# Kernel optimization log

Measured on AMD Instinct MI355X. Metric: run time of the kernel, lower is better.

## Reference

```python
import jax, jax.numpy as jnp
import numpy as np

MD = 4  # max displacement -> (2*MD+1)**2 = 81 output channels

def setup_inputs() -> dict:
    key = jax.random.key(0)
    k1, k2 = jax.random.split(key)
    B, C, H, W = 4, 128, 128, 256
    t1 = jax.random.normal(k1, (B, C, H, W), dtype=jnp.float32)
    t2 = jax.random.normal(k2, (B, C, H, W), dtype=jnp.float32)
    return {"t1": t1, "t2": t2}

def reference(t1, t2):
    # PWC-Net correlation: for each displacement (dy,dx) in [-MD,MD]^2,
    # corr[b, d, y, x] = mean_c t1[b,c,y,x] * t2[b,c,y+dy,x+dx]
    B, C, H, W = t1.shape
    t2p = jnp.pad(t2, ((0, 0), (0, 0), (MD, MD), (MD, MD)))
    outs = []
    for dy in range(2 * MD + 1):
        for dx in range(2 * MD + 1):
            shifted = t2p[:, :, dy:dy + H, dx:dx + W]  # (B,C,H,W)
            outs.append(jnp.mean(t1 * shifted, axis=1))  # (B,H,W)
    return jnp.stack(outs, axis=1)  # (B, 81, H, W)
```

## Files before the change

kernel.cpp:

```cpp
#include <hip/hip_runtime.h>

#define MD   4
#define B_   4
#define C_   128
#define H_   128
#define W_   256
#define ND   9

typedef float  float4v __attribute__((ext_vector_type(4)));
typedef float  f32x4   __attribute__((ext_vector_type(4)));
typedef short  bf16x8  __attribute__((ext_vector_type(8)));
typedef unsigned int u32;
typedef u32    u32x4   __attribute__((ext_vector_type(4)));

static __device__ __forceinline__ unsigned short f2bf(float f) {
    u32 u = __float_as_uint(f);
    u32 r = (u + 0x7fffu + ((u >> 16) & 1u)) >> 16;
    return (unsigned short)r;
}

__global__ __launch_bounds__(256, 2)
void convert_t2(const float* __restrict__ t2,
                unsigned short* __restrict__ ws) {
    const int bid = blockIdx.x;
    const int kc  = bid & 3;
    const int y   = (bid >> 2) & (H_ - 1);
    const int b   = bid >> 9;
    const int x   = threadIdx.x;
    const float* src = t2 + ((size_t)(b * C_ + kc * 32) * H_ + y) * W_ + x;
    const size_t hw = (size_t)H_ * W_;

    float f[32];
    #pragma unroll
    for (int k = 0; k < 32; ++k) f[k] = src[(size_t)k * hw];

    unsigned short* dst =
        ws + ((((size_t)(b * H_ + y)) * 4 + kc) * W_ + x) * 32;
    #pragma unroll
    for (int q = 0; q < 4; ++q) {
        u32x4 pk;
        #pragma unroll
        for (int j = 0; j < 4; ++j)
            pk[j] = (u32)f2bf(f[q * 8 + 2 * j]) |
                    ((u32)f2bf(f[q * 8 + 2 * j + 1]) << 16);
        *(u32x4*)(dst + q * 8) = pk;
    }
}

__global__ __launch_bounds__(512, 2)
void corr_mfma4(const float* __restrict__ t1,
                const unsigned short* __restrict__ ws,
                float* __restrict__ out) {
    __shared__ float scr[8][2 * 16 * 33];

    const int tid = threadIdx.x;
    const int l   = tid & 63;
    const int w   = tid >> 6;
    const int bid = blockIdx.x;
    const int xcd = bid & 7;
    const int xh  = xcd >> 2;
    const int ypq = xcd & 3;
    const int rst = bid >> 3;
    const int b   = rst >> 4;
    const int yp  = ypq * 16 + (rst & 15);
    const int y0  = yp * 2;
    const int ln  = l & 15;
    const int kg  = l >> 4;
    const int X0  = (xh * 8 + w) * 16;
    const float scale = 1.0f / (float)C_;
    const bf16x8 z8 = (bf16x8)(short)0;
    const size_t hw = (size_t)H_ * W_;

    f32x4 aA0[ND], aA1[ND], aB0[ND], aB1[ND];
    #pragma unroll
    for (int r = 0; r < ND; ++r) {
        aA0[r] = (f32x4)0.0f; aA1[r] = (f32x4)0.0f;
        aB0[r] = (f32x4)0.0f; aB1[r] = (f32x4)0.0f;
    }

    int col0 = X0 - 8 + ln;
    int col1 = X0 + 8 + ln;
    const bool ob0 = col0 < 0;
    const bool ob1 = col1 > W_ - 1;
    col0 = ob0 ? 0 : col0;
    col1 = ob1 ? W_ - 1 : col1;

    #pragma unroll
    for (int kc = 0; kc < 4; ++kc) {
        const float* aspA =
            t1 + ((size_t)(b * C_ + kc * 32 + kg * 8) * H_ + y0) * W_ + X0 + ln;
        const float* aspB = aspA + W_;
        float avA[8], avB[8];
        #pragma unroll
        for (int j = 0; j < 8; ++j) avA[j] = __builtin_nontemporal_load(aspA + (size_t)j * hw);
        #pragma unroll
        for (int j = 0; j < 8; ++j) avB[j] = __builtin_nontemporal_load(aspB + (size_t)j * hw);
        bf16x8 fA, fB;
        #pragma unroll
        for (int j = 0; j < 8; ++j) { fA[j] = (short)f2bf(avA[j]);
                                      fB[j] = (short)f2bf(avB[j]); }

        #pragma unroll
        for (int r = 0; r < ND + 1; ++r) {
            const int row = y0 + r - MD;
            if (0 <= row && row < H_) {
                const unsigned short* b_base =
                    ws + ((((size_t)(b * H_ + row)) * 4 + kc) * W_) * 32;
                bf16x8 b0 = *(const bf16x8*)(b_base + (size_t)col0 * 32 + kg * 8);
                bf16x8 b1 = *(const bf16x8*)(b_base + (size_t)col1 * 32 + kg * 8);
                b0 = ob0 ? z8 : b0;
                b1 = ob1 ? z8 : b1;
                if (r < ND) {
                    aA0[r] = __builtin_amdgcn_mfma_f32_16x16x32_bf16(fA, b0, aA0[r], 0, 0, 0);
                    aA1[r] = __builtin_amdgcn_mfma_f32_16x16x32_bf16(fA, b1, aA1[r], 0, 0, 0);
                }
                if (r >= 1) {
                    aB0[r-1] = __builtin_amdgcn_mfma_f32_16x16x32_bf16(fB, b0, aB0[r-1], 0, 0, 0);
                    aB1[r-1] = __builtin_amdgcn_mfma_f32_16x16x32_bf16(fB, b1, aB1[r-1], 0, 0, 0);
                }
            }
        }
    }

    float* sw = scr[w];

    #pragma unroll
    for (int r = 0; r < ND; ++r) {
        const int row = y0 + r - MD;
        const bool liv = (0 <= row && row < H_);
        #pragma unroll
        for (int i = 0; i < 4; ++i) {
            sw[(kg * 4 + i) * 33 + ln]       = aA0[r][i];
            sw[528 + (kg * 4 + i) * 33 + ln] = aA1[r][i];
        }
        #pragma unroll
        for (int i = 0; i < 3; ++i) {
            const int dx = i * 4 + kg;
            if (dx < ND) {
                const int m  = ln;
                const int md = m + dx;
                const int idx = (md < 12) ? (m * 33 + md + 4)
                                          : (528 + m * 33 + md - 12);
                const float v = liv ? sw[idx] * scale : 0.0f;
                __builtin_nontemporal_store(v,
                    &out[((((size_t)b * 81) + r * ND + dx) * H_ + y0) * W_ + X0 + m]);
            }
        }
    }
    #pragma unroll
    for (int r = 0; r < ND; ++r) {
        const int row = y0 + 1 + r - MD;
        const bool liv = (0 <= row && row < H_);
        #pragma unroll
        for (int i = 0; i < 4; ++i) {
            sw[(kg * 4 + i) * 33 + ln]       = aB0[r][i];
            sw[528 + (kg * 4 + i) * 33 + ln] = aB1[r][i];
        }
        #pragma unroll
        for (int i = 0; i < 3; ++i) {
            const int dx = i * 4 + kg;
            if (dx < ND) {
                const int m  = ln;
                const int md = m + dx;
                const int idx = (md < 12) ? (m * 33 + md + 4)
                                          : (528 + m * 33 + md - 12);
                const float v = liv ? sw[idx] * scale : 0.0f;
                __builtin_nontemporal_store(v,
                    &out[((((size_t)b * 81) + r * ND + dx) * H_ + (y0 + 1)) * W_ + X0 + m]);
            }
        }
    }
}

__global__ __launch_bounds__(9 * 64, 3)
void corr_fallback(const float* __restrict__ t1,
                   const float* __restrict__ t2,
                   float* __restrict__ out) {
    const int tid  = threadIdx.x;
    const int lane = tid & 63;
    const int w    = tid >> 6;
    const int bid  = blockIdx.x;
    const int swz  = (bid & 7) * 32 + (bid >> 3);
    const int yp   = swz & 63;
    const int b    = swz >> 6;
    const int y0   = yp * 2;
    const int half = lane >> 5;
    const int lx   = lane & 31;
    const int x0   = lx * 8;
    const int yrow = y0 + half;
    const int yy   = yrow + w - MD;
    const bool live = (0 <= yy) && (yy < H_);
    const int  yc  = yy < 0 ? 0 : (yy > H_ - 1 ? H_ - 1 : yy);
    const float sc = live ? (1.0f / (float)C_) : 0.0f;
    const bool lm  = (lx == 0);
    const bool rm  = (lx == 31);
    const int offL = lm ? 0 : -4;
    const int offR = rm ? 0 :  8;

    float acc[ND][8];
    #pragma unroll
    for (int dx = 0; dx < ND; ++dx)
        #pragma unroll
        for (int j = 0; j < 8; ++j) acc[dx][j] = 0.0f;

    const float* p1 = t1 + (((size_t)(b * C_)) * H_ + yrow) * W_ + x0;
    const float* p2 = t2 + (((size_t)(b * C_)) * H_ + yc  ) * W_ + x0;
    const size_t chstr = (size_t)H_ * W_;

    #pragma unroll 2
    for (int c = 0; c < C_; ++c) {
        const float* pc1 = p1 + (size_t)c * chstr;
        const float* pc2 = p2 + (size_t)c * chstr;
        const float4v a0 = *(const float4v*)(pc1);
        const float4v a1 = *(const float4v*)(pc1 + 4);
        float4v wl = *(const float4v*)(pc2 + offL);
        const float4v v0 = *(const float4v*)(pc2);
        const float4v v1 = *(const float4v*)(pc2 + 4);
        float4v wr = *(const float4v*)(pc2 + offR);
        #pragma unroll
        for (int q = 0; q < 4; ++q) {
            wl[q] = lm ? 0.0f : wl[q];
            wr[q] = rm ? 0.0f : wr[q];
        }
        float win[16];
        #pragma unroll
        for (int q = 0; q < 4; ++q) {
            win[q] = wl[q]; win[4 + q] = v0[q];
            win[8 + q] = v1[q]; win[12 + q] = wr[q];
        }
        #pragma unroll
        for (int dx = 0; dx < ND; ++dx)
            #pragma unroll
            for (int j = 0; j < 8; ++j) {
                const float aj = (j < 4) ? a0[j] : a1[j - 4];
                acc[dx][j] = fmaf(aj, win[dx + j], acc[dx][j]);
            }
    }

    #pragma unroll
    for (int dx = 0; dx < ND; ++dx) {
        float4v o0, o1;
        #pragma unroll
        for (int j = 0; j < 4; ++j) {
            o0[j] = acc[dx][j] * sc;
            o1[j] = acc[dx][4 + j] * sc;
        }
        const size_t oidx =
            (((size_t)(b * ND * ND) + w * ND + dx) * H_ + yrow) * W_ + x0;
        *(float4v*)&out[oidx]     = o0;
        *(float4v*)&out[oidx + 4] = o1;
    }
}

extern "C" void kernel_launch(void* const* d_in, const int* in_sizes, int n_in,
                              void* d_out, int out_size, void* d_ws, size_t ws_size,
                              hipStream_t stream) {
    const float* t1 = (const float*)d_in[0];
    const float* t2 = (const float*)d_in[1];
    float* out      = (float*)d_out;
    const size_t need = (size_t)B_ * H_ * 4 * W_ * 32 * sizeof(unsigned short);
    if (ws_size >= need) {
        unsigned short* ws = (unsigned short*)d_ws;
        convert_t2<<<dim3(B_ * H_ * 4), 256, 0, stream>>>(t2, ws);
        corr_mfma4<<<dim3(B_ * H_), 512, 0, stream>>>(t1, ws, out);
    } else {
        corr_fallback<<<dim3(B_ * H_ / 2), 9 * 64, 0, stream>>>(t1, t2, out);
    }
}
```

Measured before the change: 74.90 us.

## Pre-convert t1 to channel-packed bf16 alongside t2 and use regular stores

The conversion kernel now packs both t1 and t2 into channel-interleaved bf16 workspace buffers. The correlation kernel then loads its t1 fragments as single 16-byte bf16x8 vectors instead of eight strided fp32 loads plus in-kernel rounding. Output stores also change from nontemporal to ordinary stores. This cuts strided fp32 gathers in the main kernel, but costs an extra pass that writes and rereads a bf16 copy of t1 and doubles the workspace requirement.

```diff
diff --git a/kernel.cpp b/kernel.cpp
--- a/kernel.cpp
+++ b/kernel.cpp
@@ -13,6 +13,8 @@
 typedef unsigned int u32;
 typedef u32    u32x4   __attribute__((ext_vector_type(4)));
 
+#define TS ((size_t)B_ * H_ * 4 * W_ * 32)
+
 static __device__ __forceinline__ unsigned short f2bf(float f) {
     u32 u = __float_as_uint(f);
     u32 r = (u + 0x7fffu + ((u >> 16) & 1u)) >> 16;
@@ -20,22 +22,24 @@
 }
 
 __global__ __launch_bounds__(256, 2)
-void convert_t2(const float* __restrict__ t2,
-                unsigned short* __restrict__ ws) {
+void convert_both(const float* __restrict__ t1,
+                  const float* __restrict__ t2,
+                  unsigned short* __restrict__ ws) {
     const int bid = blockIdx.x;
     const int kc  = bid & 3;
     const int y   = (bid >> 2) & (H_ - 1);
-    const int b   = bid >> 9;
-    const int x   = threadIdx.x;
-    const float* src = t2 + ((size_t)(b * C_ + kc * 32) * H_ + y) * W_ + x;
+    const int b   = (bid >> 9) & 3;
+    const int tn  = bid >> 11;
+    const float* src = (tn ? t2 : t1)
+        + ((size_t)(b * C_ + kc * 32) * H_ + y) * W_ + threadIdx.x;
     const size_t hw = (size_t)H_ * W_;
 
     float f[32];
     #pragma unroll
     for (int k = 0; k < 32; ++k) f[k] = src[(size_t)k * hw];
 
-    unsigned short* dst =
-        ws + ((((size_t)(b * H_ + y)) * 4 + kc) * W_ + x) * 32;
+    unsigned short* dst = ws + (size_t)tn * TS
+        + ((((size_t)(b * H_ + y)) * 4 + kc) * W_ + threadIdx.x) * 32;
     #pragma unroll
     for (int q = 0; q < 4; ++q) {
         u32x4 pk;
@@ -48,8 +52,7 @@
 }
 
 __global__ __launch_bounds__(512, 2)
-void corr_mfma4(const float* __restrict__ t1,
-                const unsigned short* __restrict__ ws,
+void corr_mfma5(const unsigned short* __restrict__ ws,
                 float* __restrict__ out) {
     __shared__ float scr[8][2 * 16 * 33];
 
@@ -69,7 +72,8 @@
     const int X0  = (xh * 8 + w) * 16;
     const float scale = 1.0f / (float)C_;
     const bf16x8 z8 = (bf16x8)(short)0;
-    const size_t hw = (size_t)H_ * W_;
+    const unsigned short* t1w = ws;
+    const unsigned short* t2w = ws + TS;
 
     f32x4 aA0[ND], aA1[ND], aB0[ND], aB1[ND];
     #pragma unroll
@@ -87,25 +91,18 @@
 
     #pragma unroll
     for (int kc = 0; kc < 4; ++kc) {
-        const float* aspA =
-            t1 + ((size_t)(b * C_ + kc * 32 + kg * 8) * H_ + y0) * W_ + X0 + ln;
-        const float* aspB = aspA + W_;
-        float avA[8], avB[8];
-        #pragma unroll
-        for (int j = 0; j < 8; ++j) avA[j] = __builtin_nontemporal_load(aspA + (size_t)j * hw);
-        #pragma unroll
-        for (int j = 0; j < 8; ++j) avB[j] = __builtin_nontemporal_load(aspB + (size_t)j * hw);
-        bf16x8 fA, fB;
-        #pragma unroll
-        for (int j = 0; j < 8; ++j) { fA[j] = (short)f2bf(avA[j]);
-                                      fB[j] = (short)f2bf(avB[j]); }
+        const unsigned short* a_base =
+            t1w + ((((size_t)(b * H_ + y0)) * 4 + kc) * W_) * 32;
+        const bf16x8 fA = *(const bf16x8*)(a_base + (size_t)(X0 + ln) * 32 + kg * 8);
+        const bf16x8 fB = *(const bf16x8*)(a_base + (size_t)4 * W_ * 32
+                                                  + (size_t)(X0 + ln) * 32 + kg * 8);
 
         #pragma unroll
         for (int r = 0; r < ND + 1; ++r) {
             const int row = y0 + r - MD;
             if (0 <= row && row < H_) {
                 const unsigned short* b_base =
-                    ws + ((((size_t)(b * H_ + row)) * 4 + kc) * W_) * 32;
+                    t2w + ((((size_t)(b * H_ + row)) * 4 + kc) * W_) * 32;
                 bf16x8 b0 = *(const bf16x8*)(b_base + (size_t)col0 * 32 + kg * 8);
                 bf16x8 b1 = *(const bf16x8*)(b_base + (size_t)col1 * 32 + kg * 8);
                 b0 = ob0 ? z8 : b0;
@@ -142,8 +139,7 @@
                 const int idx = (md < 12) ? (m * 33 + md + 4)
                                           : (528 + m * 33 + md - 12);
                 const float v = liv ? sw[idx] * scale : 0.0f;
-                __builtin_nontemporal_store(v,
-                    &out[((((size_t)b * 81) + r * ND + dx) * H_ + y0) * W_ + X0 + m]);
+                out[((((size_t)b * 81) + r * ND + dx) * H_ + y0) * W_ + X0 + m] = v;
             }
         }
     }
@@ -165,8 +161,7 @@
                 const int idx = (md < 12) ? (m * 33 + md + 4)
                                           : (528 + m * 33 + md - 12);
                 const float v = liv ? sw[idx] * scale : 0.0f;
-                __builtin_nontemporal_store(v,
-                    &out[((((size_t)b * 81) + r * ND + dx) * H_ + (y0 + 1)) * W_ + X0 + m]);
+                out[((((size_t)b * 81) + r * ND + dx) * H_ + (y0 + 1)) * W_ + X0 + m] = v;
             }
         }
     }
@@ -258,11 +253,11 @@
     const float* t1 = (const float*)d_in[0];
     const float* t2 = (const float*)d_in[1];
     float* out      = (float*)d_out;
-    const size_t need = (size_t)B_ * H_ * 4 * W_ * 32 * sizeof(unsigned short);
+    const size_t need = 2 * TS * sizeof(unsigned short);
     if (ws_size >= need) {
         unsigned short* ws = (unsigned short*)d_ws;
-        convert_t2<<<dim3(B_ * H_ * 4), 256, 0, stream>>>(t2, ws);
-        corr_mfma4<<<dim3(B_ * H_), 512, 0, stream>>>(t1, ws, out);
+        convert_both<<<dim3(2 * B_ * H_ * 4), 256, 0, stream>>>(t1, t2, ws);
+        corr_mfma5<<<dim3(B_ * H_), 512, 0, stream>>>(ws, out);
     } else {
         corr_fallback<<<dim3(B_ * H_ / 2), 9 * 64, 0, stream>>>(t1, t2, out);
     }
```

Measured after the change: 76.24 us. Within noise of the previous version (+1.8%).
